# Kernel optimization log

Measured on AMD Instinct MI355X. Metric: run time of the kernel, lower is better.

## Reference

```python
import jax, jax.numpy as jnp
import numpy as np

N, E, F_IN, HID, EMB, G = 100000, 1600000, 128, 128, 128, 64


def setup_inputs() -> dict:
    key = jax.random.key(0)
    ks = jax.random.split(key, 8)
    x = jax.random.normal(ks[0], (N, F_IN), jnp.float32)
    edge_index = jax.random.randint(ks[1], (2, E), 0, N, dtype=jnp.int64)
    batch = jnp.sort(jax.random.randint(ks[2], (N,), 0, G, dtype=jnp.int64))
    s1 = 1.0 / np.sqrt(F_IN)
    s2 = 1.0 / np.sqrt(HID)
    W1 = jax.random.uniform(ks[3], (F_IN, HID), jnp.float32, -s1, s1)
    b1 = jnp.zeros((HID,), jnp.float32)
    W2 = jax.random.uniform(ks[4], (HID, HID), jnp.float32, -s2, s2)
    b2 = jnp.zeros((HID,), jnp.float32)
    Wp = jax.random.uniform(ks[5], (HID, EMB), jnp.float32, -s2, s2)
    bp = jax.random.uniform(ks[6], (EMB,), jnp.float32, -s2, s2)
    return dict(x=x, edge_index=edge_index, batch=batch,
                W1=W1, b1=b1, W2=W2, b2=b2, Wp=Wp, bp=bp)


def _gcn_norm(edge_index, num_nodes):
    # PyG GCNConv: add self-loops, symmetric normalization D^-1/2 (A+I) D^-1/2
    loops = jnp.arange(num_nodes, dtype=edge_index.dtype)
    row = jnp.concatenate([edge_index[0], loops])  # sources
    col = jnp.concatenate([edge_index[1], loops])  # targets
    deg = jax.ops.segment_sum(jnp.ones_like(col, jnp.float32), col, num_segments=num_nodes)
    dis = jnp.where(deg > 0, jax.lax.rsqrt(jnp.maximum(deg, 1.0)), 0.0)
    norm = dis[row] * dis[col]  # [E + N]
    return row, col, norm


def reference(x, edge_index, batch, W1, b1, W2, b2, Wp, bp):
    n = x.shape[0]
    row, col, norm = _gcn_norm(edge_index, n)

    def gcn(h, W, b):
        h = h @ W                                   # [N, HID] small GEMM
        msg = h[row] * norm[:, None]                # gather + scale [E+N, HID]
        return jax.ops.segment_sum(msg, col, num_segments=n) + b  # scatter-add

    h = jax.nn.relu(gcn(x, W1, b1))   # dropout p=0.2 is identity in eval mode
    h = jax.nn.relu(gcn(h, W2, b2))
    # global_mean_pool over graph ids
    cnt = jax.ops.segment_sum(jnp.ones((n,), jnp.float32), batch, num_segments=G)
    pooled = jax.ops.segment_sum(h, batch, num_segments=G) / jnp.maximum(cnt, 1.0)[:, None]
    return pooled @ Wp + bp  # [G, EMB]
```

## Files before the change

kernel.cpp:

```cpp
#include <hip/hip_runtime.h>
#include <cstdint>
#include <cstddef>

#define GG 64
#define EPB 4096
#define BUK_SHIFT 9
#define BUK_NODES 512
#define BCAP 16384
#define PCHUNK 64
#define NCH 8

typedef unsigned int uint;
typedef unsigned short ushort;
typedef __attribute__((ext_vector_type(8))) short short8v;
typedef __attribute__((ext_vector_type(4))) float f32x4;

__device__ __forceinline__ float blo(uint u) { return __uint_as_float(u << 16); }
__device__ __forceinline__ float bhi(uint u) { return __uint_as_float(u & 0xffff0000u); }

__device__ __forceinline__ uint bf16rne(float f) {
  uint u = __float_as_uint(f);
  return (u + 0x7fffu + ((u >> 16) & 1u)) >> 16;
}


__global__ __launch_bounds__(256) void initcur_kernel(int* __restrict__ gcur) {
  gcur[threadIdx.x] = threadIdx.x * BCAP;
}

__global__ __launch_bounds__(256) void bin_kernel(const int* __restrict__ row,
                                                  const int* __restrict__ col,
                                                  int* __restrict__ gcur,
                                                  uint* __restrict__ binned, int E) {
  __shared__ int h[256];
  __shared__ int bbase[256];
  __shared__ int lcur[256];
  const int tid = threadIdx.x;
  const int base = blockIdx.x * EPB;
  int src[EPB / 256];
  int dst[EPB / 256];
#pragma unroll
  for (int j = 0; j < EPB / 256; ++j) {
    int e = base + j * 256 + tid;
    if (e < E) {
      src[j] = row[e];
      dst[j] = col[e];
    } else {
      dst[j] = -1;
    }
  }
  h[tid] = 0;
  lcur[tid] = 0;
  __syncthreads();
#pragma unroll
  for (int j = 0; j < EPB / 256; ++j)
    if (dst[j] >= 0) atomicAdd(&h[dst[j] >> BUK_SHIFT], 1);
  __syncthreads();
  if (h[tid] > 0) bbase[tid] = atomicAdd(&gcur[tid], h[tid]);
  __syncthreads();
#pragma unroll
  for (int j = 0; j < EPB / 256; ++j) {
    if (dst[j] >= 0) {
      int b = dst[j] >> BUK_SHIFT;
      int r = atomicAdd(&lcur[b], 1);
      int pos = bbase[b] + r;
      if (pos < ((b + 1) * BCAP))
        binned[pos] = (uint)src[j] | ((uint)(dst[j] & (BUK_NODES - 1)) << 17);
    }
  }
}

__global__ __launch_bounds__(256) void build_kernel(const uint* __restrict__ binned,
                                                    const int* __restrict__ gcur,
                                                    int2* __restrict__ ndesc,
                                                    float* __restrict__ dis,
                                                    int* __restrict__ csr, int n) {
  __shared__ int h[BUK_NODES * NCH];
  __shared__ int off[BUK_NODES * NCH];
  __shared__ int ps[256];
  const int tid = threadIdx.x;
  const int b = blockIdx.x;
  const int lo = b * BCAP;
  const int hi = min(gcur[b], lo + BCAP);
#pragma unroll
  for (int k = tid; k < BUK_NODES * NCH; k += 256) h[k] = 0;
  __syncthreads();
  for (int i = lo + tid; i < hi; i += 256) {
    uint u = binned[i];
    int key = (int)((u >> 17) << 3) | (int)((u & 0x1FFFFu) >> 14);
    atomicAdd(&h[key], 1);
  }
  __syncthreads();
  const int b16 = tid * 16;
  int loc[16];
  int s = 0;
#pragma unroll
  for (int j = 0; j < 16; ++j) {
    loc[j] = s;
    s += h[b16 + j];
  }
  ps[tid] = s;
  __syncthreads();
  for (int o = 1; o < 256; o <<= 1) {
    int t = 0;
    if (tid >= o) t = ps[tid - o];
    __syncthreads();
    ps[tid] += t;
    __syncthreads();
  }
  const int excl = ps[tid] - s;
#pragma unroll
  for (int j = 0; j < 16; ++j) off[b16 + j] = excl + loc[j];
  __syncthreads();
  const int node0 = b << BUK_SHIFT;
  for (int k = tid; k < BUK_NODES; k += 256) {
    int node = node0 + k;
    if (node < n) {
      int deg = 0;
#pragma unroll
      for (int c = 0; c < NCH; ++c) deg += h[k * NCH + c];
      dis[node] = rsqrtf((float)(deg + 1));
      int e0 = lo + off[k * NCH];
      int e1 = (k == BUK_NODES - 1) ? hi : lo + off[(k + 1) * NCH];
      ndesc[node] = make_int2(e0, e1);
    }
  }
  __syncthreads();
  for (int i = lo + tid; i < hi; i += 256) {
    uint u = binned[i];
    int key = (int)((u >> 17) << 3) | (int)((u & 0x1FFFFu) >> 14);
    int s2 = (int)(u & 0x1FFFFu);
    int r = atomicAdd(&off[key], 1);
    csr[lo + r] = s2;
  }
}


__global__ __launch_bounds__(256) void wconv_kernel(const float* __restrict__ W1,
                                                    const float* __restrict__ W2,
                                                    ushort* __restrict__ Whi1,
                                                    ushort* __restrict__ Wlo1,
                                                    ushort* __restrict__ Whi2,
                                                    ushort* __restrict__ Wlo2) {
  const int g = blockIdx.x;
  const float* W = (g < 8) ? W1 : W2;
  ushort* Whi = (g < 8) ? Whi1 : Whi2;
  ushort* Wlo = (g < 8) ? Wlo1 : Wlo2;
  int slot = (g & 7) * 256 + threadIdx.x;
  int lane = slot & 63;
  int j = (slot >> 6) & 7;
  int kc = slot >> 9;
  ushort hb[8], lb[8];
#pragma unroll
  for (int i = 0; i < 8; ++i) {
    int k = kc * 32 + ((lane >> 4) << 3) + i;
    int c = j * 16 + (lane & 15);
    float f = W[k * 128 + c];
    uint hi = bf16rne(f);
    float hif = __uint_as_float(hi << 16);
    uint lo = __float_as_uint(f - hif) >> 16;
    hb[i] = (ushort)hi;
    lb[i] = (ushort)lo;
  }
  *reinterpret_cast<uint4*>(Whi + (size_t)slot * 8) = *reinterpret_cast<uint4*>(hb);
  *reinterpret_cast<uint4*>(Wlo + (size_t)slot * 8) = *reinterpret_cast<uint4*>(lb);
}


template <bool ABF16>
__global__ __launch_bounds__(256) void gemm_mfma(const void* __restrict__ Ain,
                                                 const ushort* __restrict__ Whi,
                                                 const ushort* __restrict__ Wlo,
                                                 const float* __restrict__ scale,
                                                 uint* __restrict__ Cb, int n) {
  const int tid = threadIdx.x;
  const int wave = tid >> 6, lane = tid & 63;
  const int row = blockIdx.x * 64 + wave * 16 + (lane & 15);
  const int kgrp = lane >> 4;
  const bool rowok = row < n;

  f32x4 acc[8];
#pragma unroll
  for (int j = 0; j < 8; ++j) acc[j] = (f32x4){0.f, 0.f, 0.f, 0.f};

#pragma unroll
  for (int kc = 0; kc < 4; ++kc) {
    short8v ahi, alo;
    if constexpr (ABF16) {
      if (rowok) {
        ahi = *reinterpret_cast<const short8v*>(
            (const ushort*)Ain + (size_t)row * 128 + kc * 32 + kgrp * 8);
      } else {
#pragma unroll
        for (int i = 0; i < 8; ++i) ahi[i] = 0;
      }
    } else {
      const float* ap = (const float*)Ain + (size_t)row * 128 + kc * 32 + kgrp * 8;
      float4 a0 = make_float4(0.f, 0.f, 0.f, 0.f), a1 = a0;
      if (rowok) {
        a0 = *reinterpret_cast<const float4*>(ap);
        a1 = *reinterpret_cast<const float4*>(ap + 4);
      }
#pragma unroll
      for (int i = 0; i < 8; ++i) {
        float f = (i < 4) ? (&a0.x)[i] : (&a1.x)[i - 4];
        uint hi = bf16rne(f);
        float hif = __uint_as_float(hi << 16);
        uint lo = __float_as_uint(f - hif) >> 16;
        ahi[i] = (short)hi;
        alo[i] = (short)lo;
      }
    }
#pragma unroll
    for (int j = 0; j < 8; ++j) {
      const size_t base = ((size_t)(kc * 8 + j) * 64 + lane) * 8;
      short8v whi = *reinterpret_cast<const short8v*>(Whi + base);
      short8v wlo = *reinterpret_cast<const short8v*>(Wlo + base);
      acc[j] = __builtin_amdgcn_mfma_f32_16x16x32_bf16(whi, ahi, acc[j], 0, 0, 0);
      if constexpr (!ABF16)
        acc[j] = __builtin_amdgcn_mfma_f32_16x16x32_bf16(whi, alo, acc[j], 0, 0, 0);
      acc[j] = __builtin_amdgcn_mfma_f32_16x16x32_bf16(wlo, ahi, acc[j], 0, 0, 0);
    }
  }

  if (rowok) {
    const float s = scale[row];
#pragma unroll
    for (int j = 0; j < 8; ++j) {
      uint u0 = bf16rne(acc[j][0] * s) | (bf16rne(acc[j][1] * s) << 16);
      uint u1 = bf16rne(acc[j][2] * s) | (bf16rne(acc[j][3] * s) << 16);
      *reinterpret_cast<uint2*>(Cb + (size_t)row * 64 + j * 8 + kgrp * 2) =
          make_uint2(u0, u1);
    }
  }
}


__global__ __launch_bounds__(256) void agg_kernel(const uint* __restrict__ T,
                                                  const int2* __restrict__ ndesc,
                                                  const int* __restrict__ csr,
                                                  const float* __restrict__ dis,
                                                  const float* __restrict__ bias,
                                                  uint* __restrict__ O, int n) {
  int wid = (blockIdx.x << 2) + (threadIdx.x >> 6);
  if (wid >= n) return;
  wid = __builtin_amdgcn_readfirstlane(wid);
  const int lane = threadIdx.x & 63;
  const int sub = lane & 15;
  const int grp = lane >> 4;
  const uint4* T4 = reinterpret_cast<const uint4*>(T) + sub;
  const int2 dd = ndesc[wid];
  const float di = dis[wid];

  float acc[8];
#pragma unroll
  for (int j = 0; j < 8; ++j) acc[j] = 0.f;

#define ACC8(g)                          \
  do {                                   \
    acc[0] += blo((g).x);                \
    acc[1] += bhi((g).x);                \
    acc[2] += blo((g).y);                \
    acc[3] += bhi((g).y);                \
    acc[4] += blo((g).z);                \
    acc[5] += bhi((g).z);                \
    acc[6] += blo((g).w);                \
    acc[7] += bhi((g).w);                \
  } while (0)

  for (int base = dd.x; base < dd.y; base += 64) {
    const int cn = min(64, dd.y - base);
    const int sv = (lane < cn) ? csr[base + lane] : 0;
    int e = 0;
    for (; e + 16 <= cn; e += 16) {
      int s0 = __shfl(sv, e + grp, 64);
      int s1 = __shfl(sv, e + 4 + grp, 64);
      int s2 = __shfl(sv, e + 8 + grp, 64);
      int s3 = __shfl(sv, e + 12 + grp, 64);
      uint4 g0 = T4[(size_t)s0 * 16];
      uint4 g1 = T4[(size_t)s1 * 16];
      uint4 g2 = T4[(size_t)s2 * 16];
      uint4 g3 = T4[(size_t)s3 * 16];
      ACC8(g0);
      ACC8(g1);
      ACC8(g2);
      ACC8(g3);
    }
    for (; e < cn; e += 4) {
      int ei = e + grp;
      int s = __shfl(sv, (ei < cn) ? ei : 0, 64);
      uint4 g = T4[(size_t)s * 16];
      if (ei < cn) ACC8(g);
    }
  }
#pragma unroll
  for (int j = 0; j < 8; ++j) {
    acc[j] += __shfl_xor(acc[j], 16, 64);
    acc[j] += __shfl_xor(acc[j], 32, 64);
  }
  uint4 us = T4[(size_t)wid * 16];
  float4 b0 = *reinterpret_cast<const float4*>(bias + sub * 8);
  float4 b1 = *reinterpret_cast<const float4*>(bias + sub * 8 + 4);
  float o0 = fmaxf(fmaf(di, acc[0] + blo(us.x), b0.x), 0.f);
  float o1 = fmaxf(fmaf(di, acc[1] + bhi(us.x), b0.y), 0.f);
  float o2 = fmaxf(fmaf(di, acc[2] + blo(us.y), b0.z), 0.f);
  float o3 = fmaxf(fmaf(di, acc[3] + bhi(us.y), b0.w), 0.f);
  float o4 = fmaxf(fmaf(di, acc[4] + blo(us.z), b1.x), 0.f);
  float o5 = fmaxf(fmaf(di, acc[5] + bhi(us.z), b1.y), 0.f);
  float o6 = fmaxf(fmaf(di, acc[6] + blo(us.w), b1.z), 0.f);
  float o7 = fmaxf(fmaf(di, acc[7] + bhi(us.w), b1.w), 0.f);
  if (grp == 0) {
    uint4 ov;
    ov.x = bf16rne(o0) | (bf16rne(o1) << 16);
    ov.y = bf16rne(o2) | (bf16rne(o3) << 16);
    ov.z = bf16rne(o4) | (bf16rne(o5) << 16);
    ov.w = bf16rne(o6) | (bf16rne(o7) << 16);
    reinterpret_cast<uint4*>(O)[(size_t)wid * 16 + sub] = ov;
  }
#undef ACC8
}


__global__ __launch_bounds__(256) void pool_kernel(const uint* __restrict__ H,
                                                   const int* __restrict__ batch,
                                                   float* __restrict__ pooled,
                                                   float* __restrict__ cntg, int n) {
  __shared__ float sd[256 * 4];
  const int tid = threadIdx.x;
  const int c4 = (tid & 31) << 2;
  const int rs = tid >> 5;
  const int base = blockIdx.x * PCHUNK;
  const int lim = min(base + PCHUNK, n);
  const int g0 = batch[base];
  const int gN = batch[lim - 1];
  float4 acc = make_float4(0.f, 0.f, 0.f, 0.f);
  if (g0 == gN) {
    for (int r = base + rs; r < lim; r += 8) {
      uint2 v = *reinterpret_cast<const uint2*>(H + (size_t)r * 64 + (c4 >> 1));
      acc.x += blo(v.x); acc.y += bhi(v.x); acc.z += blo(v.y); acc.w += bhi(v.y);
    }
    *reinterpret_cast<float4*>(&sd[tid * 4]) = acc;
    __syncthreads();
    if (tid < 128) {
      float4 o = *reinterpret_cast<float4*>(&sd[(tid + 128) * 4]);
      acc.x += o.x; acc.y += o.y; acc.z += o.z; acc.w += o.w;
      *reinterpret_cast<float4*>(&sd[tid * 4]) = acc;
    }
    __syncthreads();
    if (tid < 64) {
      float4 o = *reinterpret_cast<float4*>(&sd[(tid + 64) * 4]);
      acc.x += o.x; acc.y += o.y; acc.z += o.z; acc.w += o.w;
      *reinterpret_cast<float4*>(&sd[tid * 4]) = acc;
    }
    __syncthreads();
    if (tid < 32) {
      float4 o = *reinterpret_cast<float4*>(&sd[(tid + 32) * 4]);
      acc.x += o.x; acc.y += o.y; acc.z += o.z; acc.w += o.w;
      atomicAdd(&pooled[g0 * 128 + c4 + 0], acc.x);
      atomicAdd(&pooled[g0 * 128 + c4 + 1], acc.y);
      atomicAdd(&pooled[g0 * 128 + c4 + 2], acc.z);
      atomicAdd(&pooled[g0 * 128 + c4 + 3], acc.w);
      if (tid == 0) atomicAdd(&cntg[g0], (float)(lim - base));
    }
  } else {
    int curg = -1, cnt = 0;
    for (int r = base + rs; r < lim; r += 8) {
      int g = batch[r];
      if (g != curg) {
        if (curg >= 0) {
          atomicAdd(&pooled[curg * 128 + c4 + 0], acc.x);
          atomicAdd(&pooled[curg * 128 + c4 + 1], acc.y);
          atomicAdd(&pooled[curg * 128 + c4 + 2], acc.z);
          atomicAdd(&pooled[curg * 128 + c4 + 3], acc.w);
          if ((tid & 31) == 0) atomicAdd(&cntg[curg], (float)cnt);
        }
        curg = g;
        acc = make_float4(0.f, 0.f, 0.f, 0.f);
        cnt = 0;
      }
      uint2 v = *reinterpret_cast<const uint2*>(H + (size_t)r * 64 + (c4 >> 1));
      acc.x += blo(v.x); acc.y += bhi(v.x); acc.z += blo(v.y); acc.w += bhi(v.y);
      cnt++;
    }
    if (curg >= 0) {
      atomicAdd(&pooled[curg * 128 + c4 + 0], acc.x);
      atomicAdd(&pooled[curg * 128 + c4 + 1], acc.y);
      atomicAdd(&pooled[curg * 128 + c4 + 2], acc.z);
      atomicAdd(&pooled[curg * 128 + c4 + 3], acc.w);
      if ((tid & 31) == 0) atomicAdd(&cntg[curg], (float)cnt);
    }
  }
}

__global__ __launch_bounds__(128) void final_kernel(const float* __restrict__ pooled,
                                                    const float* __restrict__ cntg,
                                                    const float* __restrict__ Wp,
                                                    const float* __restrict__ bp,
                                                    float* __restrict__ out) {
  const int g = blockIdx.x;
  const int e = threadIdx.x;
  float inv = 1.0f / fmaxf(cntg[g], 1.0f);
  float acc = 0.f;
  for (int c = 0; c < 128; ++c)
    acc = fmaf(pooled[g * 128 + c], Wp[c * 128 + e], acc);
  out[g * 128 + e] = acc * inv + bp[e];
}


extern "C" void kernel_launch(void* const* d_in, const int* in_sizes, int n_in,
                              void* d_out, int out_size, void* d_ws, size_t ws_size,
                              hipStream_t stream) {
  const float* x = (const float*)d_in[0];
  const int* eidx = (const int*)d_in[1];
  const int* batch = (const int*)d_in[2];
  const float* W1 = (const float*)d_in[3];
  const float* b1 = (const float*)d_in[4];
  const float* W2 = (const float*)d_in[5];
  const float* b2 = (const float*)d_in[6];
  const float* Wp = (const float*)d_in[7];
  const float* bp = (const float*)d_in[8];

  const int n = in_sizes[0] / 128;
  const int E = in_sizes[1] / 2;
  const int* row = eidx;
  const int* col = eidx + E;
  const int nbuk = (n + BUK_NODES - 1) >> BUK_SHIFT;

  char* ws = (char*)d_ws;
  size_t off = 0;
  auto alloc = [&](size_t bytes) {
    void* p = ws + off;
    off = (off + bytes + 255) & ~(size_t)255;
    return p;
  };
  uint* Tb = (uint*)alloc((size_t)n * 64 * 4);
  uint* Bb = (uint*)alloc((size_t)n * 64 * 4);
  float* dis = (float*)alloc((size_t)n * 4);
  int2* ndesc = (int2*)alloc((size_t)n * 8);
  int* csr = (int*)alloc((size_t)nbuk * BCAP * 4);
  uint* binned = (uint*)alloc((size_t)nbuk * BCAP * 4);
  int* gcur = (int*)alloc(256 * 4);
  float* zbase = (float*)alloc((64 + GG * 128) * 4);
  float* cntg = zbase;
  float* pooled = zbase + 64;
  ushort* Whi1 = (ushort*)alloc(2048 * 8 * 2);
  ushort* Wlo1 = (ushort*)alloc(2048 * 8 * 2);
  ushort* Whi2 = (ushort*)alloc(2048 * 8 * 2);
  ushort* Wlo2 = (ushort*)alloc(2048 * 8 * 2);
  (void)off;

  hipMemsetAsync(zbase, 0, (64 + GG * 128) * 4, stream);
  initcur_kernel<<<1, 256, 0, stream>>>(gcur);

  const int eblocks = (E + EPB - 1) / EPB;
  bin_kernel<<<eblocks, 256, 0, stream>>>(row, col, gcur, binned, E);
  build_kernel<<<nbuk, 256, 0, stream>>>(binned, gcur, ndesc, dis, csr, n);
  wconv_kernel<<<16, 256, 0, stream>>>(W1, W2, Whi1, Wlo1, Whi2, Wlo2);

  const int gblocks = (n + 63) / 64;
  gemm_mfma<false><<<gblocks, 256, 0, stream>>>(x, Whi1, Wlo1, dis, Tb, n);
  agg_kernel<<<(n + 3) / 4, 256, 0, stream>>>(Tb, ndesc, csr, dis, b1, Bb, n);
  gemm_mfma<true><<<gblocks, 256, 0, stream>>>(Bb, Whi2, Wlo2, dis, Tb, n);
  agg_kernel<<<(n + 3) / 4, 256, 0, stream>>>(Tb, ndesc, csr, dis, b2, Bb, n);

  pool_kernel<<<(n + PCHUNK - 1) / PCHUNK, 256, 0, stream>>>(Bb, batch, pooled, cntg, n);
  final_kernel<<<GG, 128, 0, stream>>>(pooled, cntg, Wp, bp, (float*)d_out);
}
```

Baseline: 258.3 us.

## Fuse second aggregation with mean pooling and merge setup kernels

The second GCN aggregation now accumulates its ReLU output straight into per-graph pooled sums, using shared-memory partials and global atomics, so the Bb write and the separate pool pass are gone. Weight conversion, cursor init and the per-graph node counts are merged into one setup kernel. The CSR build drops the 8-way source-chunk sub-bucketing, which used to order edges by source within each node, in favour of a plain per-node histogram. Risks include more atomics, since each wave handles 4 nodes serially, and a less cache-friendly gather order.

New measurement: 279.1 us. 1.08x slower.

```diff
diff --git a/kernel.cpp b/kernel.cpp
--- a/kernel.cpp
+++ b/kernel.cpp
@@ -7,8 +7,6 @@
 #define BUK_SHIFT 9
 #define BUK_NODES 512
 #define BCAP 16384
-#define PCHUNK 64
-#define NCH 8
 
 typedef unsigned int uint;
 typedef unsigned short ushort;
@@ -24,9 +22,57 @@
 }
 
 
-__global__ __launch_bounds__(256) void initcur_kernel(int* __restrict__ gcur) {
-  gcur[threadIdx.x] = threadIdx.x * BCAP;
-}
+__global__ __launch_bounds__(256) void setup_kernel(const float* __restrict__ W1,
+                                                    const float* __restrict__ W2,
+                                                    ushort* __restrict__ Whi1,
+                                                    ushort* __restrict__ Wlo1,
+                                                    ushort* __restrict__ Whi2,
+                                                    ushort* __restrict__ Wlo2,
+                                                    int* __restrict__ gcur,
+                                                    const int* __restrict__ batch,
+                                                    float* __restrict__ cntg, int n) {
+  const int b = blockIdx.x;
+  const int tid = threadIdx.x;
+  if (b == 0) {
+    gcur[tid] = tid * BCAP;
+    return;
+  }
+  if (b <= 16) {
+    const int g = b - 1;
+    const float* W = (g < 8) ? W1 : W2;
+    ushort* Whi = (g < 8) ? Whi1 : Whi2;
+    ushort* Wlo = (g < 8) ? Wlo1 : Wlo2;
+    int slot = (g & 7) * 256 + tid;
+    int lane = slot & 63;
+    int j = (slot >> 6) & 7;
+    int kc = slot >> 9;
+    ushort hb[8], lb[8];
+#pragma unroll
+    for (int i = 0; i < 8; ++i) {
+      int k = kc * 32 + ((lane >> 4) << 3) + i;
+      int c = j * 16 + (lane & 15);
+      float f = W[k * 128 + c];
+      uint hi = bf16rne(f);
+      float hif = __uint_as_float(hi << 16);
+      uint lo = __float_as_uint(f - hif) >> 16;
+      hb[i] = (ushort)hi;
+      lb[i] = (ushort)lo;
+    }
+    *reinterpret_cast<uint4*>(Whi + (size_t)slot * 8) = *reinterpret_cast<uint4*>(hb);
+    *reinterpret_cast<uint4*>(Wlo + (size_t)slot * 8) = *reinterpret_cast<uint4*>(lb);
+    return;
+  }
+  __shared__ int hb2[GG];
+  const int bk = b - 17;
+  const int seg = (n + 63) >> 6;
+  const int lo = bk * seg, hi = min(n, lo + seg);
+  if (tid < GG) hb2[tid] = 0;
+  __syncthreads();
+  for (int i = lo + tid; i < hi; i += 256) atomicAdd(&hb2[batch[i]], 1);
+  __syncthreads();
+  if (tid < GG && hb2[tid]) atomicAdd(&cntg[tid], (float)hb2[tid]);
+}
+
 
 __global__ __launch_bounds__(256) void bin_kernel(const int* __restrict__ row,
                                                   const int* __restrict__ col,
@@ -75,31 +121,20 @@
                                                     int2* __restrict__ ndesc,
                                                     float* __restrict__ dis,
                                                     int* __restrict__ csr, int n) {
-  __shared__ int h[BUK_NODES * NCH];
-  __shared__ int off[BUK_NODES * NCH];
+  __shared__ int h[BUK_NODES];
+  __shared__ int off2[BUK_NODES];
   __shared__ int ps[256];
   const int tid = threadIdx.x;
   const int b = blockIdx.x;
   const int lo = b * BCAP;
   const int hi = min(gcur[b], lo + BCAP);
-#pragma unroll
-  for (int k = tid; k < BUK_NODES * NCH; k += 256) h[k] = 0;
-  __syncthreads();
-  for (int i = lo + tid; i < hi; i += 256) {
-    uint u = binned[i];
-    int key = (int)((u >> 17) << 3) | (int)((u & 0x1FFFFu) >> 14);
-    atomicAdd(&h[key], 1);
-  }
-  __syncthreads();
-  const int b16 = tid * 16;
-  int loc[16];
-  int s = 0;
-#pragma unroll
-  for (int j = 0; j < 16; ++j) {
-    loc[j] = s;
-    s += h[b16 + j];
-  }
-  ps[tid] = s;
+  h[tid] = 0;
+  h[tid + 256] = 0;
+  __syncthreads();
+  for (int i = lo + tid; i < hi; i += 256) atomicAdd(&h[binned[i] >> 17], 1);
+  __syncthreads();
+  int a0 = h[2 * tid], a1 = h[2 * tid + 1];
+  ps[tid] = a0 + a1;
   __syncthreads();
   for (int o = 1; o < 256; o <<= 1) {
     int t = 0;
@@ -108,62 +143,26 @@
     ps[tid] += t;
     __syncthreads();
   }
-  const int excl = ps[tid] - s;
-#pragma unroll
-  for (int j = 0; j < 16; ++j) off[b16 + j] = excl + loc[j];
+  int pexcl = ps[tid] - (a0 + a1);
+  off2[2 * tid] = pexcl;
+  off2[2 * tid + 1] = pexcl + a0;
   __syncthreads();
   const int node0 = b << BUK_SHIFT;
   for (int k = tid; k < BUK_NODES; k += 256) {
     int node = node0 + k;
     if (node < n) {
-      int deg = 0;
-#pragma unroll
-      for (int c = 0; c < NCH; ++c) deg += h[k * NCH + c];
+      int deg = h[k];
       dis[node] = rsqrtf((float)(deg + 1));
-      int e0 = lo + off[k * NCH];
-      int e1 = (k == BUK_NODES - 1) ? hi : lo + off[(k + 1) * NCH];
-      ndesc[node] = make_int2(e0, e1);
+      int e0 = lo + off2[k];
+      ndesc[node] = make_int2(e0, e0 + deg);
     }
   }
   __syncthreads();
   for (int i = lo + tid; i < hi; i += 256) {
     uint u = binned[i];
-    int key = (int)((u >> 17) << 3) | (int)((u & 0x1FFFFu) >> 14);
-    int s2 = (int)(u & 0x1FFFFu);
-    int r = atomicAdd(&off[key], 1);
-    csr[lo + r] = s2;
-  }
-}
-
-
-__global__ __launch_bounds__(256) void wconv_kernel(const float* __restrict__ W1,
-                                                    const float* __restrict__ W2,
-                                                    ushort* __restrict__ Whi1,
-                                                    ushort* __restrict__ Wlo1,
-                                                    ushort* __restrict__ Whi2,
-                                                    ushort* __restrict__ Wlo2) {
-  const int g = blockIdx.x;
-  const float* W = (g < 8) ? W1 : W2;
-  ushort* Whi = (g < 8) ? Whi1 : Whi2;
-  ushort* Wlo = (g < 8) ? Wlo1 : Wlo2;
-  int slot = (g & 7) * 256 + threadIdx.x;
-  int lane = slot & 63;
-  int j = (slot >> 6) & 7;
-  int kc = slot >> 9;
-  ushort hb[8], lb[8];
-#pragma unroll
-  for (int i = 0; i < 8; ++i) {
-    int k = kc * 32 + ((lane >> 4) << 3) + i;
-    int c = j * 16 + (lane & 15);
-    float f = W[k * 128 + c];
-    uint hi = bf16rne(f);
-    float hif = __uint_as_float(hi << 16);
-    uint lo = __float_as_uint(f - hif) >> 16;
-    hb[i] = (ushort)hi;
-    lb[i] = (ushort)lo;
-  }
-  *reinterpret_cast<uint4*>(Whi + (size_t)slot * 8) = *reinterpret_cast<uint4*>(hb);
-  *reinterpret_cast<uint4*>(Wlo + (size_t)slot * 8) = *reinterpret_cast<uint4*>(lb);
+    int r = atomicAdd(&off2[u >> 17], 1);
+    csr[lo + r] = (int)(u & 0x1FFFFu);
+  }
 }
 
 
@@ -236,38 +235,23 @@
 }
 
 
-__global__ __launch_bounds__(256) void agg_kernel(const uint* __restrict__ T,
-                                                  const int2* __restrict__ ndesc,
-                                                  const int* __restrict__ csr,
-                                                  const float* __restrict__ dis,
-                                                  const float* __restrict__ bias,
-                                                  uint* __restrict__ O, int n) {
-  int wid = (blockIdx.x << 2) + (threadIdx.x >> 6);
-  if (wid >= n) return;
-  wid = __builtin_amdgcn_readfirstlane(wid);
-  const int lane = threadIdx.x & 63;
-  const int sub = lane & 15;
-  const int grp = lane >> 4;
+__device__ __forceinline__ void gather_row(const uint* __restrict__ T,
+                                           const int* __restrict__ csr,
+                                           const int2 dd, const int lane,
+                                           const int grp, const int sub,
+                                           float acc[8]) {
   const uint4* T4 = reinterpret_cast<const uint4*>(T) + sub;
-  const int2 dd = ndesc[wid];
-  const float di = dis[wid];
-
-  float acc[8];
-#pragma unroll
-  for (int j = 0; j < 8; ++j) acc[j] = 0.f;
-
-#define ACC8(g)                          \
-  do {                                   \
-    acc[0] += blo((g).x);                \
-    acc[1] += bhi((g).x);                \
-    acc[2] += blo((g).y);                \
-    acc[3] += bhi((g).y);                \
-    acc[4] += blo((g).z);                \
-    acc[5] += bhi((g).z);                \
-    acc[6] += blo((g).w);                \
-    acc[7] += bhi((g).w);                \
+#define ACC8(g)           \
+  do {                    \
+    acc[0] += blo((g).x); \
+    acc[1] += bhi((g).x); \
+    acc[2] += blo((g).y); \
+    acc[3] += bhi((g).y); \
+    acc[4] += blo((g).z); \
+    acc[5] += bhi((g).z); \
+    acc[6] += blo((g).w); \
+    acc[7] += bhi((g).w); \
   } while (0)
-
   for (int base = dd.x; base < dd.y; base += 64) {
     const int cn = min(64, dd.y - base);
     const int sv = (lane < cn) ? csr[base + lane] : 0;
@@ -293,11 +277,34 @@
       if (ei < cn) ACC8(g);
     }
   }
+#undef ACC8
+}
+
+__global__ __launch_bounds__(256) void agg_kernel(const uint* __restrict__ T,
+                                                  const int2* __restrict__ ndesc,
+                                                  const int* __restrict__ csr,
+                                                  const float* __restrict__ dis,
+                                                  const float* __restrict__ bias,
+                                                  uint* __restrict__ O, int n) {
+  int wid = (blockIdx.x << 2) + (threadIdx.x >> 6);
+  if (wid >= n) return;
+  wid = __builtin_amdgcn_readfirstlane(wid);
+  const int lane = threadIdx.x & 63;
+  const int sub = lane & 15;
+  const int grp = lane >> 4;
+  const int2 dd = ndesc[wid];
+  const float di = dis[wid];
+
+  float acc[8];
+#pragma unroll
+  for (int j = 0; j < 8; ++j) acc[j] = 0.f;
+  gather_row(T, csr, dd, lane, grp, sub, acc);
 #pragma unroll
   for (int j = 0; j < 8; ++j) {
     acc[j] += __shfl_xor(acc[j], 16, 64);
     acc[j] += __shfl_xor(acc[j], 32, 64);
   }
+  const uint4* T4 = reinterpret_cast<const uint4*>(T) + sub;
   uint4 us = T4[(size_t)wid * 16];
   float4 b0 = *reinterpret_cast<const float4*>(bias + sub * 8);
   float4 b1 = *reinterpret_cast<const float4*>(bias + sub * 8 + 4);
@@ -317,80 +324,81 @@
     ov.w = bf16rne(o6) | (bf16rne(o7) << 16);
     reinterpret_cast<uint4*>(O)[(size_t)wid * 16 + sub] = ov;
   }
-#undef ACC8
-}
-
-
-__global__ __launch_bounds__(256) void pool_kernel(const uint* __restrict__ H,
-                                                   const int* __restrict__ batch,
-                                                   float* __restrict__ pooled,
-                                                   float* __restrict__ cntg, int n) {
-  __shared__ float sd[256 * 4];
+}
+
+__global__ __launch_bounds__(256) void agg_pool_kernel(const uint* __restrict__ T,
+                                                       const int2* __restrict__ ndesc,
+                                                       const int* __restrict__ csr,
+                                                       const float* __restrict__ dis,
+                                                       const float* __restrict__ bias,
+                                                       const int* __restrict__ batch,
+                                                       float* __restrict__ pooled,
+                                                       int n) {
+  __shared__ float pacc[2][128];
   const int tid = threadIdx.x;
-  const int c4 = (tid & 31) << 2;
-  const int rs = tid >> 5;
-  const int base = blockIdx.x * PCHUNK;
-  const int lim = min(base + PCHUNK, n);
-  const int g0 = batch[base];
-  const int gN = batch[lim - 1];
-  float4 acc = make_float4(0.f, 0.f, 0.f, 0.f);
-  if (g0 == gN) {
-    for (int r = base + rs; r < lim; r += 8) {
-      uint2 v = *reinterpret_cast<const uint2*>(H + (size_t)r * 64 + (c4 >> 1));
-      acc.x += blo(v.x); acc.y += bhi(v.x); acc.z += blo(v.y); acc.w += bhi(v.y);
-    }
-    *reinterpret_cast<float4*>(&sd[tid * 4]) = acc;
-    __syncthreads();
-    if (tid < 128) {
-      float4 o = *reinterpret_cast<float4*>(&sd[(tid + 128) * 4]);
-      acc.x += o.x; acc.y += o.y; acc.z += o.z; acc.w += o.w;
-      *reinterpret_cast<float4*>(&sd[tid * 4]) = acc;
-    }
-    __syncthreads();
-    if (tid < 64) {
-      float4 o = *reinterpret_cast<float4*>(&sd[(tid + 64) * 4]);
-      acc.x += o.x; acc.y += o.y; acc.z += o.z; acc.w += o.w;
-      *reinterpret_cast<float4*>(&sd[tid * 4]) = acc;
-    }
-    __syncthreads();
-    if (tid < 32) {
-      float4 o = *reinterpret_cast<float4*>(&sd[(tid + 32) * 4]);
-      acc.x += o.x; acc.y += o.y; acc.z += o.z; acc.w += o.w;
-      atomicAdd(&pooled[g0 * 128 + c4 + 0], acc.x);
-      atomicAdd(&pooled[g0 * 128 + c4 + 1], acc.y);
-      atomicAdd(&pooled[g0 * 128 + c4 + 2], acc.z);
-      atomicAdd(&pooled[g0 * 128 + c4 + 3], acc.w);
-      if (tid == 0) atomicAdd(&cntg[g0], (float)(lim - base));
-    }
-  } else {
-    int curg = -1, cnt = 0;
-    for (int r = base + rs; r < lim; r += 8) {
-      int g = batch[r];
-      if (g != curg) {
-        if (curg >= 0) {
-          atomicAdd(&pooled[curg * 128 + c4 + 0], acc.x);
-          atomicAdd(&pooled[curg * 128 + c4 + 1], acc.y);
-          atomicAdd(&pooled[curg * 128 + c4 + 2], acc.z);
-          atomicAdd(&pooled[curg * 128 + c4 + 3], acc.w);
-          if ((tid & 31) == 0) atomicAdd(&cntg[curg], (float)cnt);
-        }
-        curg = g;
-        acc = make_float4(0.f, 0.f, 0.f, 0.f);
-        cnt = 0;
-      }
-      uint2 v = *reinterpret_cast<const uint2*>(H + (size_t)r * 64 + (c4 >> 1));
-      acc.x += blo(v.x); acc.y += bhi(v.x); acc.z += blo(v.y); acc.w += bhi(v.y);
-      cnt++;
-    }
-    if (curg >= 0) {
-      atomicAdd(&pooled[curg * 128 + c4 + 0], acc.x);
-      atomicAdd(&pooled[curg * 128 + c4 + 1], acc.y);
-      atomicAdd(&pooled[curg * 128 + c4 + 2], acc.z);
-      atomicAdd(&pooled[curg * 128 + c4 + 3], acc.w);
-      if ((tid & 31) == 0) atomicAdd(&cntg[curg], (float)cnt);
-    }
-  }
-}
+  const int wave = tid >> 6, lane = tid & 63;
+  const int sub = lane & 15;
+  const int grp = lane >> 4;
+  const int blockBase = blockIdx.x << 4;
+  pacc[tid >> 7][tid & 127] = 0.f;
+  const int gbase = batch[blockBase];
+  __syncthreads();
+
+  const float4 b0 = *reinterpret_cast<const float4*>(bias + sub * 8);
+  const float4 b1 = *reinterpret_cast<const float4*>(bias + sub * 8 + 4);
+
+  for (int j4 = 0; j4 < 4; ++j4) {
+    const int node = blockBase + wave * 4 + j4;
+    if (node < n) {
+      const int2 dd = ndesc[node];
+      const float di = dis[node];
+      float acc[8];
+#pragma unroll
+      for (int j = 0; j < 8; ++j) acc[j] = 0.f;
+      gather_row(T, csr, dd, lane, grp, sub, acc);
+#pragma unroll
+      for (int j = 0; j < 8; ++j) {
+        acc[j] += __shfl_xor(acc[j], 16, 64);
+        acc[j] += __shfl_xor(acc[j], 32, 64);
+      }
+      const uint4* T4 = reinterpret_cast<const uint4*>(T) + sub;
+      uint4 us = T4[(size_t)node * 16];
+      float o0 = fmaxf(fmaf(di, acc[0] + blo(us.x), b0.x), 0.f);
+      float o1 = fmaxf(fmaf(di, acc[1] + bhi(us.x), b0.y), 0.f);
+      float o2 = fmaxf(fmaf(di, acc[2] + blo(us.y), b0.z), 0.f);
+      float o3 = fmaxf(fmaf(di, acc[3] + bhi(us.y), b0.w), 0.f);
+      float o4 = fmaxf(fmaf(di, acc[4] + blo(us.z), b1.x), 0.f);
+      float o5 = fmaxf(fmaf(di, acc[5] + bhi(us.z), b1.y), 0.f);
+      float o6 = fmaxf(fmaf(di, acc[6] + blo(us.w), b1.z), 0.f);
+      float o7 = fmaxf(fmaf(di, acc[7] + bhi(us.w), b1.w), 0.f);
+      float oA, oB;
+      if (grp == 0) {
+        oA = o0; oB = o1;
+      } else if (grp == 1) {
+        oA = o2; oB = o3;
+      } else if (grp == 2) {
+        oA = o4; oB = o5;
+      } else {
+        oA = o6; oB = o7;
+      }
+      const int f0 = sub * 8 + grp * 2;
+      const int g = batch[node];
+      const int idx = g - gbase;
+      if (idx < 2) {
+        atomicAdd(&pacc[idx][f0], oA);
+        atomicAdd(&pacc[idx][f0 + 1], oB);
+      } else {
+        atomicAdd(&pooled[g * 128 + f0], oA);
+        atomicAdd(&pooled[g * 128 + f0 + 1], oB);
+      }
+    }
+  }
+  __syncthreads();
+  const int fi = tid & 127, gi = gbase + (tid >> 7);
+  float v = pacc[tid >> 7][fi];
+  if (v != 0.f && gi < GG) atomicAdd(&pooled[gi * 128 + fi], v);
+}
+
 
 __global__ __launch_bounds__(128) void final_kernel(const float* __restrict__ pooled,
                                                     const float* __restrict__ cntg,
@@ -450,19 +458,18 @@
   (void)off;
 
   hipMemsetAsync(zbase, 0, (64 + GG * 128) * 4, stream);
-  initcur_kernel<<<1, 256, 0, stream>>>(gcur);
+  setup_kernel<<<81, 256, 0, stream>>>(W1, W2, Whi1, Wlo1, Whi2, Wlo2, gcur, batch,
+                                       cntg, n);
 
   const int eblocks = (E + EPB - 1) / EPB;
   bin_kernel<<<eblocks, 256, 0, stream>>>(row, col, gcur, binned, E);
   build_kernel<<<nbuk, 256, 0, stream>>>(binned, gcur, ndesc, dis, csr, n);
-  wconv_kernel<<<16, 256, 0, stream>>>(W1, W2, Whi1, Wlo1, Whi2, Wlo2);
 
   const int gblocks = (n + 63) / 64;
   gemm_mfma<false><<<gblocks, 256, 0, stream>>>(x, Whi1, Wlo1, dis, Tb, n);
   agg_kernel<<<(n + 3) / 4, 256, 0, stream>>>(Tb, ndesc, csr, dis, b1, Bb, n);
   gemm_mfma<true><<<gblocks, 256, 0, stream>>>(Bb, Whi2, Wlo2, dis, Tb, n);
-  agg_kernel<<<(n + 3) / 4, 256, 0, stream>>>(Tb, ndesc, csr, dis, b2, Bb, n);
-
-  pool_kernel<<<(n + PCHUNK - 1) / PCHUNK, 256, 0, stream>>>(Bb, batch, pooled, cntg, n);
+  agg_pool_kernel<<<(n + 15) / 16, 256, 0, stream>>>(Tb, ndesc, csr, dis, b2, batch,
+                                                     pooled, n);
   final_kernel<<<GG, 128, 0, stream>>>(pooled, cntg, Wp, bp, (float*)d_out);
 }
```

## Merge setup kernels, simplify CSR build histogram, move graph counts out of pooling

Applied to the files above, without the earlier changes.

Folds the bucket-cursor init and the weight bf16 split into a single setup kernel, which also computes per-graph node counts through a shared-memory histogram over batch ids. The CSR build now keys its histogram on destination node only, dropping the 8-way source-chunk sub-binning. That shrinks shared memory and the scan, but edges inside a node's adjacency list are no longer grouped by source range. The pool kernel no longer does count atomics, and the agg gather loop is moved into a helper function. The aim is fewer launches and cheaper CSR building, at the risk of less cache-friendly gather order during aggregation.

After: 250.4 us. 3.1% less time.

```diff
diff --git a/kernel.cpp b/kernel.cpp
--- a/kernel.cpp
+++ b/kernel.cpp
@@ -8,7 +8,6 @@
 #define BUK_NODES 512
 #define BCAP 16384
 #define PCHUNK 64
-#define NCH 8
 
 typedef unsigned int uint;
 typedef unsigned short ushort;
@@ -24,9 +23,57 @@
 }
 
 
-__global__ __launch_bounds__(256) void initcur_kernel(int* __restrict__ gcur) {
-  gcur[threadIdx.x] = threadIdx.x * BCAP;
-}
+__global__ __launch_bounds__(256) void setup_kernel(const float* __restrict__ W1,
+                                                    const float* __restrict__ W2,
+                                                    ushort* __restrict__ Whi1,
+                                                    ushort* __restrict__ Wlo1,
+                                                    ushort* __restrict__ Whi2,
+                                                    ushort* __restrict__ Wlo2,
+                                                    int* __restrict__ gcur,
+                                                    const int* __restrict__ batch,
+                                                    float* __restrict__ cntg, int n) {
+  const int b = blockIdx.x;
+  const int tid = threadIdx.x;
+  if (b == 0) {
+    gcur[tid] = tid * BCAP;
+    return;
+  }
+  if (b <= 16) {
+    const int g = b - 1;
+    const float* W = (g < 8) ? W1 : W2;
+    ushort* Whi = (g < 8) ? Whi1 : Whi2;
+    ushort* Wlo = (g < 8) ? Wlo1 : Wlo2;
+    int slot = (g & 7) * 256 + tid;
+    int lane = slot & 63;
+    int j = (slot >> 6) & 7;
+    int kc = slot >> 9;
+    ushort hb[8], lb[8];
+#pragma unroll
+    for (int i = 0; i < 8; ++i) {
+      int k = kc * 32 + ((lane >> 4) << 3) + i;
+      int c = j * 16 + (lane & 15);
+      float f = W[k * 128 + c];
+      uint hi = bf16rne(f);
+      float hif = __uint_as_float(hi << 16);
+      uint lo = __float_as_uint(f - hif) >> 16;
+      hb[i] = (ushort)hi;
+      lb[i] = (ushort)lo;
+    }
+    *reinterpret_cast<uint4*>(Whi + (size_t)slot * 8) = *reinterpret_cast<uint4*>(hb);
+    *reinterpret_cast<uint4*>(Wlo + (size_t)slot * 8) = *reinterpret_cast<uint4*>(lb);
+    return;
+  }
+  __shared__ int hb2[GG];
+  const int bk = b - 17;
+  const int seg = (n + 63) >> 6;
+  const int lo = bk * seg, hi = min(n, lo + seg);
+  if (tid < GG) hb2[tid] = 0;
+  __syncthreads();
+  for (int i = lo + tid; i < hi; i += 256) atomicAdd(&hb2[batch[i]], 1);
+  __syncthreads();
+  if (tid < GG && hb2[tid]) atomicAdd(&cntg[tid], (float)hb2[tid]);
+}
+
 
 __global__ __launch_bounds__(256) void bin_kernel(const int* __restrict__ row,
                                                   const int* __restrict__ col,
@@ -75,31 +122,20 @@
                                                     int2* __restrict__ ndesc,
                                                     float* __restrict__ dis,
                                                     int* __restrict__ csr, int n) {
-  __shared__ int h[BUK_NODES * NCH];
-  __shared__ int off[BUK_NODES * NCH];
+  __shared__ int h[BUK_NODES];
+  __shared__ int off2[BUK_NODES];
   __shared__ int ps[256];
   const int tid = threadIdx.x;
   const int b = blockIdx.x;
   const int lo = b * BCAP;
   const int hi = min(gcur[b], lo + BCAP);
-#pragma unroll
-  for (int k = tid; k < BUK_NODES * NCH; k += 256) h[k] = 0;
-  __syncthreads();
-  for (int i = lo + tid; i < hi; i += 256) {
-    uint u = binned[i];
-    int key = (int)((u >> 17) << 3) | (int)((u & 0x1FFFFu) >> 14);
-    atomicAdd(&h[key], 1);
-  }
-  __syncthreads();
-  const int b16 = tid * 16;
-  int loc[16];
-  int s = 0;
-#pragma unroll
-  for (int j = 0; j < 16; ++j) {
-    loc[j] = s;
-    s += h[b16 + j];
-  }
-  ps[tid] = s;
+  h[tid] = 0;
+  h[tid + 256] = 0;
+  __syncthreads();
+  for (int i = lo + tid; i < hi; i += 256) atomicAdd(&h[binned[i] >> 17], 1);
+  __syncthreads();
+  int a0 = h[2 * tid], a1 = h[2 * tid + 1];
+  ps[tid] = a0 + a1;
   __syncthreads();
   for (int o = 1; o < 256; o <<= 1) {
     int t = 0;
@@ -108,62 +144,26 @@
     ps[tid] += t;
     __syncthreads();
   }
-  const int excl = ps[tid] - s;
-#pragma unroll
-  for (int j = 0; j < 16; ++j) off[b16 + j] = excl + loc[j];
+  int pexcl = ps[tid] - (a0 + a1);
+  off2[2 * tid] = pexcl;
+  off2[2 * tid + 1] = pexcl + a0;
   __syncthreads();
   const int node0 = b << BUK_SHIFT;
   for (int k = tid; k < BUK_NODES; k += 256) {
     int node = node0 + k;
     if (node < n) {
-      int deg = 0;
-#pragma unroll
-      for (int c = 0; c < NCH; ++c) deg += h[k * NCH + c];
+      int deg = h[k];
       dis[node] = rsqrtf((float)(deg + 1));
-      int e0 = lo + off[k * NCH];
-      int e1 = (k == BUK_NODES - 1) ? hi : lo + off[(k + 1) * NCH];
-      ndesc[node] = make_int2(e0, e1);
+      int e0 = lo + off2[k];
+      ndesc[node] = make_int2(e0, e0 + deg);
     }
   }
   __syncthreads();
   for (int i = lo + tid; i < hi; i += 256) {
     uint u = binned[i];
-    int key = (int)((u >> 17) << 3) | (int)((u & 0x1FFFFu) >> 14);
-    int s2 = (int)(u & 0x1FFFFu);
-    int r = atomicAdd(&off[key], 1);
-    csr[lo + r] = s2;
-  }
-}
-
-
-__global__ __launch_bounds__(256) void wconv_kernel(const float* __restrict__ W1,
-                                                    const float* __restrict__ W2,
-                                                    ushort* __restrict__ Whi1,
-                                                    ushort* __restrict__ Wlo1,
-                                                    ushort* __restrict__ Whi2,
-                                                    ushort* __restrict__ Wlo2) {
-  const int g = blockIdx.x;
-  const float* W = (g < 8) ? W1 : W2;
-  ushort* Whi = (g < 8) ? Whi1 : Whi2;
-  ushort* Wlo = (g < 8) ? Wlo1 : Wlo2;
-  int slot = (g & 7) * 256 + threadIdx.x;
-  int lane = slot & 63;
-  int j = (slot >> 6) & 7;
-  int kc = slot >> 9;
-  ushort hb[8], lb[8];
-#pragma unroll
-  for (int i = 0; i < 8; ++i) {
-    int k = kc * 32 + ((lane >> 4) << 3) + i;
-    int c = j * 16 + (lane & 15);
-    float f = W[k * 128 + c];
-    uint hi = bf16rne(f);
-    float hif = __uint_as_float(hi << 16);
-    uint lo = __float_as_uint(f - hif) >> 16;
-    hb[i] = (ushort)hi;
-    lb[i] = (ushort)lo;
-  }
-  *reinterpret_cast<uint4*>(Whi + (size_t)slot * 8) = *reinterpret_cast<uint4*>(hb);
-  *reinterpret_cast<uint4*>(Wlo + (size_t)slot * 8) = *reinterpret_cast<uint4*>(lb);
+    int r = atomicAdd(&off2[u >> 17], 1);
+    csr[lo + r] = (int)(u & 0x1FFFFu);
+  }
 }
 
 
@@ -236,38 +236,23 @@
 }
 
 
-__global__ __launch_bounds__(256) void agg_kernel(const uint* __restrict__ T,
-                                                  const int2* __restrict__ ndesc,
-                                                  const int* __restrict__ csr,
-                                                  const float* __restrict__ dis,
-                                                  const float* __restrict__ bias,
-                                                  uint* __restrict__ O, int n) {
-  int wid = (blockIdx.x << 2) + (threadIdx.x >> 6);
-  if (wid >= n) return;
-  wid = __builtin_amdgcn_readfirstlane(wid);
-  const int lane = threadIdx.x & 63;
-  const int sub = lane & 15;
-  const int grp = lane >> 4;
+__device__ __forceinline__ void gather_row(const uint* __restrict__ T,
+                                           const int* __restrict__ csr,
+                                           const int2 dd, const int lane,
+                                           const int grp, const int sub,
+                                           float acc[8]) {
   const uint4* T4 = reinterpret_cast<const uint4*>(T) + sub;
-  const int2 dd = ndesc[wid];
-  const float di = dis[wid];
-
-  float acc[8];
-#pragma unroll
-  for (int j = 0; j < 8; ++j) acc[j] = 0.f;
-
-#define ACC8(g)                          \
-  do {                                   \
-    acc[0] += blo((g).x);                \
-    acc[1] += bhi((g).x);                \
-    acc[2] += blo((g).y);                \
-    acc[3] += bhi((g).y);                \
-    acc[4] += blo((g).z);                \
-    acc[5] += bhi((g).z);                \
-    acc[6] += blo((g).w);                \
-    acc[7] += bhi((g).w);                \
+#define ACC8(g)           \
+  do {                    \
+    acc[0] += blo((g).x); \
+    acc[1] += bhi((g).x); \
+    acc[2] += blo((g).y); \
+    acc[3] += bhi((g).y); \
+    acc[4] += blo((g).z); \
+    acc[5] += bhi((g).z); \
+    acc[6] += blo((g).w); \
+    acc[7] += bhi((g).w); \
   } while (0)
-
   for (int base = dd.x; base < dd.y; base += 64) {
     const int cn = min(64, dd.y - base);
     const int sv = (lane < cn) ? csr[base + lane] : 0;
@@ -293,11 +278,34 @@
       if (ei < cn) ACC8(g);
     }
   }
+#undef ACC8
+}
+
+__global__ __launch_bounds__(256) void agg_kernel(const uint* __restrict__ T,
+                                                  const int2* __restrict__ ndesc,
+                                                  const int* __restrict__ csr,
+                                                  const float* __restrict__ dis,
+                                                  const float* __restrict__ bias,
+                                                  uint* __restrict__ O, int n) {
+  int wid = (blockIdx.x << 2) + (threadIdx.x >> 6);
+  if (wid >= n) return;
+  wid = __builtin_amdgcn_readfirstlane(wid);
+  const int lane = threadIdx.x & 63;
+  const int sub = lane & 15;
+  const int grp = lane >> 4;
+  const int2 dd = ndesc[wid];
+  const float di = dis[wid];
+
+  float acc[8];
+#pragma unroll
+  for (int j = 0; j < 8; ++j) acc[j] = 0.f;
+  gather_row(T, csr, dd, lane, grp, sub, acc);
 #pragma unroll
   for (int j = 0; j < 8; ++j) {
     acc[j] += __shfl_xor(acc[j], 16, 64);
     acc[j] += __shfl_xor(acc[j], 32, 64);
   }
+  const uint4* T4 = reinterpret_cast<const uint4*>(T) + sub;
   uint4 us = T4[(size_t)wid * 16];
   float4 b0 = *reinterpret_cast<const float4*>(bias + sub * 8);
   float4 b1 = *reinterpret_cast<const float4*>(bias + sub * 8 + 4);
@@ -317,14 +325,12 @@
     ov.w = bf16rne(o6) | (bf16rne(o7) << 16);
     reinterpret_cast<uint4*>(O)[(size_t)wid * 16 + sub] = ov;
   }
-#undef ACC8
 }
 
 
 __global__ __launch_bounds__(256) void pool_kernel(const uint* __restrict__ H,
                                                    const int* __restrict__ batch,
-                                                   float* __restrict__ pooled,
-                                                   float* __restrict__ cntg, int n) {
+                                                   float* __restrict__ pooled, int n) {
   __shared__ float sd[256 * 4];
   const int tid = threadIdx.x;
   const int c4 = (tid & 31) << 2;
@@ -360,10 +366,9 @@
       atomicAdd(&pooled[g0 * 128 + c4 + 1], acc.y);
       atomicAdd(&pooled[g0 * 128 + c4 + 2], acc.z);
       atomicAdd(&pooled[g0 * 128 + c4 + 3], acc.w);
-      if (tid == 0) atomicAdd(&cntg[g0], (float)(lim - base));
     }
   } else {
-    int curg = -1, cnt = 0;
+    int curg = -1;
     for (int r = base + rs; r < lim; r += 8) {
       int g = batch[r];
       if (g != curg) {
@@ -372,25 +377,22 @@
           atomicAdd(&pooled[curg * 128 + c4 + 1], acc.y);
           atomicAdd(&pooled[curg * 128 + c4 + 2], acc.z);
           atomicAdd(&pooled[curg * 128 + c4 + 3], acc.w);
-          if ((tid & 31) == 0) atomicAdd(&cntg[curg], (float)cnt);
         }
         curg = g;
         acc = make_float4(0.f, 0.f, 0.f, 0.f);
-        cnt = 0;
       }
       uint2 v = *reinterpret_cast<const uint2*>(H + (size_t)r * 64 + (c4 >> 1));
       acc.x += blo(v.x); acc.y += bhi(v.x); acc.z += blo(v.y); acc.w += bhi(v.y);
-      cnt++;
     }
     if (curg >= 0) {
       atomicAdd(&pooled[curg * 128 + c4 + 0], acc.x);
       atomicAdd(&pooled[curg * 128 + c4 + 1], acc.y);
       atomicAdd(&pooled[curg * 128 + c4 + 2], acc.z);
       atomicAdd(&pooled[curg * 128 + c4 + 3], acc.w);
-      if ((tid & 31) == 0) atomicAdd(&cntg[curg], (float)cnt);
-    }
-  }
-}
+    }
+  }
+}
+
 
 __global__ __launch_bounds__(128) void final_kernel(const float* __restrict__ pooled,
                                                     const float* __restrict__ cntg,
@@ -450,12 +452,12 @@
   (void)off;
 
   hipMemsetAsync(zbase, 0, (64 + GG * 128) * 4, stream);
-  initcur_kernel<<<1, 256, 0, stream>>>(gcur);
+  setup_kernel<<<81, 256, 0, stream>>>(W1, W2, Whi1, Wlo1, Whi2, Wlo2, gcur, batch,
+                                       cntg, n);
 
   const int eblocks = (E + EPB - 1) / EPB;
   bin_kernel<<<eblocks, 256, 0, stream>>>(row, col, gcur, binned, E);
   build_kernel<<<nbuk, 256, 0, stream>>>(binned, gcur, ndesc, dis, csr, n);
-  wconv_kernel<<<16, 256, 0, stream>>>(W1, W2, Whi1, Wlo1, Whi2, Wlo2);
 
   const int gblocks = (n + 63) / 64;
   gemm_mfma<false><<<gblocks, 256, 0, stream>>>(x, Whi1, Wlo1, dis, Tb, n);
@@ -463,6 +465,6 @@
   gemm_mfma<true><<<gblocks, 256, 0, stream>>>(Bb, Whi2, Wlo2, dis, Tb, n);
   agg_kernel<<<(n + 3) / 4, 256, 0, stream>>>(Tb, ndesc, csr, dis, b2, Bb, n);
 
-  pool_kernel<<<(n + PCHUNK - 1) / PCHUNK, 256, 0, stream>>>(Bb, batch, pooled, cntg, n);
+  pool_kernel<<<(n + PCHUNK - 1) / PCHUNK, 256, 0, stream>>>(Bb, batch, pooled, n);
   final_kernel<<<GG, 128, 0, stream>>>(pooled, cntg, Wp, bp, (float*)d_out);
 }
```
